# Performance work log

Hardware: AMD Instinct MI355X
Metric: run time of the kernel (lower is better)

Reference implementation:

```python
import jax, jax.numpy as jnp
import numpy as np

H = 8      # head_nums
D = 64     # head_planes
SCALE = D ** -0.5


def setup_inputs() -> dict:
    key = jax.random.key(0)
    ks = jax.random.split(key, 7)
    B, Nq, Nkv = 2, 2048, 2048
    Cq, Ck, I = 1024, 768, H * D
    return {
        "x": jax.random.normal(ks[0], (B, Nq, Cq), jnp.float32),
        "context": jax.random.normal(ks[1], (B, Nkv, Ck), jnp.float32),
        "Wq": jax.random.normal(ks[2], (Cq, I), jnp.float32) * (Cq ** -0.5),
        "Wk": jax.random.normal(ks[3], (Ck, I), jnp.float32) * (Ck ** -0.5),
        "Wv": jax.random.normal(ks[4], (Ck, I), jnp.float32) * (Ck ** -0.5),
        "Wo": jax.random.normal(ks[5], (I, Cq), jnp.float32) * (I ** -0.5),
        "bo": jnp.zeros((Cq,), jnp.float32),
    }


def reference(x, context, Wq, Wk, Wv, Wo, bo):
    B, Nq, _ = x.shape
    Nkv = context.shape[1]
    # projections (bias-free, as in to_q/to_k/to_v)
    q = (x @ Wq).reshape(B, Nq, H, D)        # b i h d
    k = (context @ Wk).reshape(B, Nkv, H, D)  # b j h d
    v = (context @ Wv).reshape(B, Nkv, H, D)
    # scaled dot-product attention, full [B,H,Nq,Nkv] scores as in original
    sim = jnp.einsum('bihd,bjhd->bhij', q, k) * SCALE
    attn = jax.nn.softmax(sim, axis=-1)
    out = jnp.einsum('bhij,bjhd->bihd', attn, v).reshape(B, Nq, H * D)
    # to_out linear (dropout_prob=0.0 -> identity)
    return out @ Wo + bo
```

## Files before the change

kernel.cpp:

```cpp
#include <hip/hip_runtime.h>
#include <hip/hip_bf16.h>

typedef __hip_bfloat16 bf16;
typedef __attribute__((ext_vector_type(8))) short short8;
typedef __attribute__((ext_vector_type(4))) float f32x4;

#define MFMA16(a, b, c) __builtin_amdgcn_mfma_f32_16x16x32_bf16((a), (b), (c), 0, 0, 0)

#define BATCH 2
#define NQ 2048
#define NKV 2048
#define HEADS 8
#define DHEAD 64
#define CQ 1024
#define CK 768
#define IDIM 512
#define SCALE 0.125f

__device__ __forceinline__ short8 ld8(const bf16* p) {
    return *(const short8*)p;
}

__device__ __forceinline__ void async_ld16(const bf16* g, bf16* l) {
    __builtin_amdgcn_global_load_lds((__attribute__((address_space(1))) const void*)g,
                                     (__attribute__((address_space(3))) void*)l,
                                     16, 0, 0);
}

__global__ __launch_bounds__(256) void prologue(
    const float* __restrict__ x, const float* __restrict__ ctx,
    const float* __restrict__ Wq, const float* __restrict__ Wk,
    const float* __restrict__ Wv, const float* __restrict__ Wo,
    bf16* __restrict__ Xb, bf16* __restrict__ Cb,
    bf16* __restrict__ WqT, bf16* __restrict__ WkT,
    bf16* __restrict__ WvT, bf16* __restrict__ WoT) {
    __shared__ float tile[64][65];
    const int t = threadIdx.x;
    const int bx = blockIdx.x;

    if (bx < 3584) {
        int idx = bx * 256 + t;
        const int NX8 = (4096 * 1024) / 8;
        const float4* srcp;
        bf16* dstp;
        if (idx < NX8) {
            srcp = (const float4*)x + (size_t)idx * 2;
            dstp = Xb + (size_t)idx * 8;
        } else {
            int j = idx - NX8;
            srcp = (const float4*)ctx + (size_t)j * 2;
            dstp = Cb + (size_t)j * 8;
        }
        float4 v0 = srcp[0], v1 = srcp[1];
        bf16 tmp[8] = {__float2bfloat16(v0.x), __float2bfloat16(v0.y),
                       __float2bfloat16(v0.z), __float2bfloat16(v0.w),
                       __float2bfloat16(v1.x), __float2bfloat16(v1.y),
                       __float2bfloat16(v1.z), __float2bfloat16(v1.w)};
        *(short8*)dstp = *(short8*)tmp;
        return;
    }

    int tb = bx - 3584;
    const float* src; bf16* dst; int R, C, ti;
    if (tb < 128)      { src = Wq; dst = WqT; R = 1024; C = 512;  ti = tb; }
    else if (tb < 224) { src = Wk; dst = WkT; R = 768;  C = 512;  ti = tb - 128; }
    else if (tb < 320) { src = Wv; dst = WvT; R = 768;  C = 512;  ti = tb - 224; }
    else               { src = Wo; dst = WoT; R = 512;  C = 1024; ti = tb - 320; }
    const int tilesC = C >> 6;
    const int tr = ti / tilesC, tc = ti - tr * tilesC;

    {
        int row = t >> 4;
        int c4 = (t & 15) * 4;
#pragma unroll
        for (int p = 0; p < 4; ++p) {
            float4 v = *(const float4*)&src[(size_t)(tr * 64 + p * 16 + row) * C + tc * 64 + c4];
            tile[p * 16 + row][c4 + 0] = v.x;
            tile[p * 16 + row][c4 + 1] = v.y;
            tile[p * 16 + row][c4 + 2] = v.z;
            tile[p * 16 + row][c4 + 3] = v.w;
        }
    }
    __syncthreads();
    {
        int oc = t >> 2;
        int r0 = (t & 3) * 16;
        bf16 tmp[16];
#pragma unroll
        for (int j = 0; j < 16; ++j)
            tmp[j] = __float2bfloat16(tile[r0 + j][oc]);
        bf16* dp = dst + (size_t)(tc * 64 + oc) * R + tr * 64 + r0;
        *(short8*)dp = *(short8*)&tmp[0];
        *(short8*)(dp + 8) = *(short8*)&tmp[8];
    }
}

__global__ __launch_bounds__(256) void qkv_gemm(
    const bf16* __restrict__ Xb, const bf16* __restrict__ Cb,
    const bf16* __restrict__ WqT, const bf16* __restrict__ WkT,
    const bf16* __restrict__ WvT,
    bf16* __restrict__ Qb, bf16* __restrict__ Kb, bf16* __restrict__ Vt) {
    __shared__ bf16 At[2][64 * 64];
    __shared__ bf16 Bts[2][128 * 64];

    const int z = blockIdx.z;
    const bf16* A  = (z == 0) ? Xb : Cb;
    const bf16* Bt = (z == 0) ? WqT : (z == 1) ? WkT : WvT;
    const int K = (z == 0) ? 1024 : 768;

    const int t = threadIdx.x;
    const int wave = t >> 6;
    const int lane = t & 63;
    const int n15 = lane & 15;
    const int quad = lane >> 4;
    const int wm = wave >> 1;
    const int wn = wave & 1;
    const int bm = blockIdx.y;
    const int bn = blockIdx.x;

    f32x4 acc[2][4] = {};

    const bf16* Ablk = A + (size_t)bm * 64 * K;
    const bf16* Bblk = Bt + (size_t)bn * 128 * K;

    int ar[2], ac[2], br[4], bc[4];
#pragma unroll
    for (int i = 0; i < 2; ++i) {
        int g = i * 256 + t;
        ar[i] = g >> 3; ac[i] = ((g & 7) ^ (ar[i] & 7)) * 8;
    }
#pragma unroll
    for (int i = 0; i < 4; ++i) {
        int g = i * 256 + t;
        br[i] = g >> 3; bc[i] = ((g & 7) ^ (br[i] & 7)) * 8;
    }

#pragma unroll
    for (int i = 0; i < 2; ++i)
        async_ld16(Ablk + ar[i] * K + ac[i], &At[0][(i * 256 + t) * 8]);
#pragma unroll
    for (int i = 0; i < 4; ++i)
        async_ld16(Bblk + br[i] * K + bc[i], &Bts[0][(i * 256 + t) * 8]);
    __syncthreads();

    for (int k0 = 0; k0 < K; k0 += 64) {
        const int p = (k0 >> 6) & 1;
        if (k0 + 64 < K) {
            const int q = p ^ 1;
            const int kn = k0 + 64;
#pragma unroll
            for (int i = 0; i < 2; ++i)
                async_ld16(Ablk + ar[i] * K + kn + ac[i], &At[q][(i * 256 + t) * 8]);
#pragma unroll
            for (int i = 0; i < 4; ++i)
                async_ld16(Bblk + br[i] * K + kn + bc[i], &Bts[q][(i * 256 + t) * 8]);
        }

#pragma unroll
        for (int kh = 0; kh < 2; ++kh) {
            short8 af[2], bfr[4];
#pragma unroll
            for (int mt = 0; mt < 2; ++mt) {
                int R = wm * 32 + mt * 16 + n15;
                af[mt] = ld8(&At[p][R * 64 + (((kh * 4 + quad) ^ (R & 7)) * 8)]);
            }
#pragma unroll
            for (int nt = 0; nt < 4; ++nt) {
                int R = wn * 64 + nt * 16 + n15;
                bfr[nt] = ld8(&Bts[p][R * 64 + (((kh * 4 + quad) ^ (R & 7)) * 8)]);
            }
#pragma unroll
            for (int mt = 0; mt < 2; ++mt)
#pragma unroll
                for (int nt = 0; nt < 4; ++nt)
                    acc[mt][nt] = MFMA16(af[mt], bfr[nt], acc[mt][nt]);
        }

        __syncthreads();
    }

    bf16* C = (z == 0) ? Qb : (z == 1) ? Kb : Vt;
#pragma unroll
    for (int mt = 0; mt < 2; ++mt) {
#pragma unroll
        for (int nt = 0; nt < 4; ++nt) {
            int col = bn * 128 + wn * 64 + nt * 16 + n15;
#pragma unroll
            for (int r = 0; r < 4; ++r) {
                int row = bm * 64 + wm * 32 + mt * 16 + quad * 4 + r;
                bf16 v = __float2bfloat16(acc[mt][nt][r]);
                if (z < 2) {
                    C[(size_t)row * 512 + col] = v;
                } else {
                    int b = row >> 11, j = row & 2047;
                    int h = col >> 6, d = col & 63;
                    C[(size_t)(((b << 3) + h) * 64 + d) * 2048 + j] = v;
                }
            }
        }
    }
}

__global__ __launch_bounds__(256) void out_gemm(const bf16* __restrict__ A,
                                                const bf16* __restrict__ Bt,
                                                const float* __restrict__ bias,
                                                float* __restrict__ C) {
    const int K = 512, N = 1024;
    __shared__ bf16 At[2][64 * 64];
    __shared__ bf16 Bts[2][128 * 64];

    const int t = threadIdx.x;
    const int wave = t >> 6;
    const int lane = t & 63;
    const int n15 = lane & 15;
    const int quad = lane >> 4;
    const int wm = wave >> 1;
    const int wn = wave & 1;
    const int bm = blockIdx.y;
    const int bn = blockIdx.x;

    f32x4 acc[2][4] = {};

    const bf16* Ablk = A + (size_t)bm * 64 * K;
    const bf16* Bblk = Bt + (size_t)bn * 128 * K;

    int ar[2], ac[2], br[4], bc[4];
#pragma unroll
    for (int i = 0; i < 2; ++i) {
        int g = i * 256 + t;
        ar[i] = g >> 3; ac[i] = ((g & 7) ^ (ar[i] & 7)) * 8;
    }
#pragma unroll
    for (int i = 0; i < 4; ++i) {
        int g = i * 256 + t;
        br[i] = g >> 3; bc[i] = ((g & 7) ^ (br[i] & 7)) * 8;
    }

#pragma unroll
    for (int i = 0; i < 2; ++i)
        async_ld16(Ablk + ar[i] * K + ac[i], &At[0][(i * 256 + t) * 8]);
#pragma unroll
    for (int i = 0; i < 4; ++i)
        async_ld16(Bblk + br[i] * K + bc[i], &Bts[0][(i * 256 + t) * 8]);
    __syncthreads();

    for (int k0 = 0; k0 < K; k0 += 64) {
        const int p = (k0 >> 6) & 1;
        if (k0 + 64 < K) {
            const int q = p ^ 1;
            const int kn = k0 + 64;
#pragma unroll
            for (int i = 0; i < 2; ++i)
                async_ld16(Ablk + ar[i] * K + kn + ac[i], &At[q][(i * 256 + t) * 8]);
#pragma unroll
            for (int i = 0; i < 4; ++i)
                async_ld16(Bblk + br[i] * K + kn + bc[i], &Bts[q][(i * 256 + t) * 8]);
        }

#pragma unroll
        for (int kh = 0; kh < 2; ++kh) {
            short8 af[2], bfr[4];
#pragma unroll
            for (int mt = 0; mt < 2; ++mt) {
                int R = wm * 32 + mt * 16 + n15;
                af[mt] = ld8(&At[p][R * 64 + (((kh * 4 + quad) ^ (R & 7)) * 8)]);
            }
#pragma unroll
            for (int nt = 0; nt < 4; ++nt) {
                int R = wn * 64 + nt * 16 + n15;
                bfr[nt] = ld8(&Bts[p][R * 64 + (((kh * 4 + quad) ^ (R & 7)) * 8)]);
            }
#pragma unroll
            for (int mt = 0; mt < 2; ++mt)
#pragma unroll
                for (int nt = 0; nt < 4; ++nt)
                    acc[mt][nt] = MFMA16(af[mt], bfr[nt], acc[mt][nt]);
        }

        __syncthreads();
    }

#pragma unroll
    for (int mt = 0; mt < 2; ++mt) {
#pragma unroll
        for (int nt = 0; nt < 4; ++nt) {
            int col = bn * 128 + wn * 64 + nt * 16 + n15;
            float bv = bias[col];
#pragma unroll
            for (int r = 0; r < 4; ++r) {
                int row = bm * 64 + wm * 32 + mt * 16 + quad * 4 + r;
                C[(size_t)row * N + col] = acc[mt][nt][r] + bv;
            }
        }
    }
}

__global__ __launch_bounds__(256, 1) void flash_attn(const bf16* __restrict__ Q,
                                                     const bf16* __restrict__ K,
                                                     const bf16* __restrict__ Vt,
                                                     bf16* __restrict__ O) {
    __shared__ bf16 Kt[2][64 * 64];
    __shared__ bf16 Vte[2][64 * 64];
    __shared__ bf16 Pa[4][32 * 72];

    const int t = threadIdx.x;
    const int wave = t >> 6;
    const int lane = t & 63;
    const int n15 = lane & 15;
    const int quad = lane >> 4;

    const int L = blockIdx.x;
    const int bh = L & 15;
    const int b = bh >> 3, h = bh & 7;
    const int q0 = (L >> 4) * 128;
    const int qw = q0 + wave * 32;

    const bf16* Qp = Q + ((size_t)(b * NQ + qw) * IDIM + h * DHEAD);
    const bf16* Kp = K + ((size_t)b * NKV * IDIM + h * DHEAD);
    const bf16* Vp = Vt + (size_t)((b * HEADS + h) * DHEAD) * NKV;
    bf16* Pw = Pa[wave];

    short8 qa[2][2];
#pragma unroll
    for (int j = 0; j < 2; ++j)
#pragma unroll
        for (int kh = 0; kh < 2; ++kh)
            qa[j][kh] = ld8(Qp + (j * 16 + n15) * IDIM + kh * 32 + quad * 8);

    const int s0 = wave * 128 + lane;
    const int s1 = s0 + 64;
    const int r0 = s0 >> 3, c0 = (s0 & 7) ^ (r0 & 7);
    const int r1 = s1 >> 3, c1 = (s1 & 7) ^ (r1 & 7);
    const bf16* kg0 = Kp + r0 * IDIM + c0 * 8;
    const bf16* kg1 = Kp + r1 * IDIM + c1 * 8;
    const bf16* vg0 = Vp + (size_t)r0 * NKV + c0 * 8;
    const bf16* vg1 = Vp + (size_t)r1 * NKV + c1 * 8;

    f32x4 o[4][2] = {};
    float lsum[2] = {0.f, 0.f};
    const int sw = n15 & 7;

    async_ld16(kg0, &Kt[0][s0 * 8]);
    async_ld16(kg1, &Kt[0][s1 * 8]);
    async_ld16(vg0, &Vte[0][s0 * 8]);
    async_ld16(vg1, &Vte[0][s1 * 8]);
    __syncthreads();

    for (int key0 = 0; key0 < NKV; key0 += 64) {
        const int p = (key0 >> 6) & 1;
        if (key0 + 64 < NKV) {
            const int q = p ^ 1;
            const int kn = key0 + 64;
            async_ld16(kg0 + (size_t)kn * IDIM, &Kt[q][s0 * 8]);
            async_ld16(kg1 + (size_t)kn * IDIM, &Kt[q][s1 * 8]);
            async_ld16(vg0 + kn, &Vte[q][s0 * 8]);
            async_ld16(vg1 + kn, &Vte[q][s1 * 8]);
        }

        f32x4 s[4][2] = {};
#pragma unroll
        for (int su = 0; su < 4; ++su) {
            const bf16* kr = &Kt[p][(su * 16 + n15) * 64];
            short8 ka0 = ld8(kr + ((quad ^ sw) * 8));
            short8 ka1 = ld8(kr + (((4 + quad) ^ sw) * 8));
#pragma unroll
            for (int j = 0; j < 2; ++j) {
                s[su][j] = MFMA16(ka0, qa[j][0], s[su][j]);
                s[su][j] = MFMA16(ka1, qa[j][1], s[su][j]);
            }
        }

#pragma unroll
        for (int su = 0; su < 4; ++su) {
#pragma unroll
            for (int j = 0; j < 2; ++j) {
                float p0 = __expf(s[su][j][0] * SCALE);
                float p1 = __expf(s[su][j][1] * SCALE);
                float p2 = __expf(s[su][j][2] * SCALE);
                float p3 = __expf(s[su][j][3] * SCALE);
                lsum[j] += (p0 + p1) + (p2 + p3);
                bf16 pk[4] = {__float2bfloat16(p0), __float2bfloat16(p1),
                              __float2bfloat16(p2), __float2bfloat16(p3)};
                *(uint2*)&Pw[(j * 16 + n15) * 72 + su * 16 + quad * 4] = *(uint2*)pk;
            }
        }
        asm volatile("s_waitcnt lgkmcnt(0)" ::: "memory");

        short8 pb[2][2];
#pragma unroll
        for (int j = 0; j < 2; ++j) {
            pb[j][0] = ld8(&Pw[(j * 16 + n15) * 72 + quad * 8]);
            pb[j][1] = ld8(&Pw[(j * 16 + n15) * 72 + 32 + quad * 8]);
        }

#pragma unroll
        for (int d4 = 0; d4 < 4; ++d4) {
            const bf16* vr = &Vte[p][(d4 * 16 + n15) * 64];
            short8 va0 = ld8(vr + ((quad ^ sw) * 8));
            short8 va1 = ld8(vr + (((4 + quad) ^ sw) * 8));
#pragma unroll
            for (int j = 0; j < 2; ++j) {
                o[d4][j] = MFMA16(va0, pb[j][0], o[d4][j]);
                o[d4][j] = MFMA16(va1, pb[j][1], o[d4][j]);
            }
        }
        __syncthreads();
    }

#pragma unroll
    for (int j = 0; j < 2; ++j) {
        float lt = lsum[j];
        lt += __shfl_xor(lt, 16, 64);
        lt += __shfl_xor(lt, 32, 64);
        float inv = 1.0f / lt;
#pragma unroll
        for (int d4 = 0; d4 < 4; ++d4) {
            bf16 pk[4];
#pragma unroll
            for (int r = 0; r < 4; ++r)
                pk[r] = __float2bfloat16(o[d4][j][r] * inv);
            *(uint2*)&Pw[(j * 16 + n15) * 72 + d4 * 16 + quad * 4] = *(uint2*)pk;
        }
    }
    __syncthreads();

    {
        int ql = t >> 1, seg = t & 1;
        const bf16* src = &Pa[ql >> 5][(ql & 31) * 72 + seg * 32];
        short8 a0 = ld8(src);
        short8 a1 = ld8(src + 8);
        short8 a2 = ld8(src + 16);
        short8 a3 = ld8(src + 24);
        bf16* dst = O + ((size_t)(b * NQ + q0 + ql) * IDIM + h * DHEAD + seg * 32);
        *(short8*)dst = a0;
        *(short8*)(dst + 8) = a1;
        *(short8*)(dst + 16) = a2;
        *(short8*)(dst + 24) = a3;
    }
}

extern "C" void kernel_launch(void* const* d_in, const int* in_sizes, int n_in,
                              void* d_out, int out_size, void* d_ws, size_t ws_size,
                              hipStream_t stream) {
    (void)in_sizes; (void)n_in; (void)out_size; (void)ws_size;

    const float* x   = (const float*)d_in[0];
    const float* ctx = (const float*)d_in[1];
    const float* Wq  = (const float*)d_in[2];
    const float* Wk  = (const float*)d_in[3];
    const float* Wv  = (const float*)d_in[4];
    const float* Wo  = (const float*)d_in[5];
    const float* bo  = (const float*)d_in[6];
    float* out = (float*)d_out;

    char* ws = (char*)d_ws;
    bf16* Xb  = (bf16*)(ws + 0);
    bf16* Cb  = (bf16*)(ws + 8388608);
    bf16* WqT = (bf16*)(ws + 14680064);
    bf16* WkT = (bf16*)(ws + 15728640);
    bf16* WvT = (bf16*)(ws + 16515072);
    bf16* WoT = (bf16*)(ws + 17301504);
    bf16* Qb  = (bf16*)(ws + 18350080);
    bf16* Kb  = (bf16*)(ws + 22544384);
    bf16* Vt  = (bf16*)(ws + 26738688);
    bf16* Ob  = (bf16*)(ws + 30932992);

    prologue<<<4032, 256, 0, stream>>>(x, ctx, Wq, Wk, Wv, Wo,
                                       Xb, Cb, WqT, WkT, WvT, WoT);

    qkv_gemm<<<dim3(4, 64, 3), 256, 0, stream>>>(Xb, Cb, WqT, WkT, WvT, Qb, Kb, Vt);

    flash_attn<<<256, 256, 0, stream>>>(Qb, Kb, Vt, Ob);

    out_gemm<<<dim3(8, 64), 256, 0, stream>>>(Ob, WoT, bo, out);
}
```

Before: 167.0 us.

## Split attention keys across wave pairs and double the flash-attention grid

Flash attention now runs 512 blocks of 512 threads. Each block covers 64 queries, and each pair of waves splits the 2048 keys into two halves. Their partial outputs and row sums are merged through shared memory before normalisation. The aim is to double the parallelism and the waves resident per CU for this small grid. The cost is losing the double-buffered K/V prefetch (each tile now loads and then synchronises), halving the reuse of each K/V fragment per wave, and adding a cross-wave reduction step.

Result: faster. 149.2 us (-10.7%).

```diff
diff --git a/kernel.cpp b/kernel.cpp
--- a/kernel.cpp
+++ b/kernel.cpp
@@ -295,16 +295,20 @@
     }
 }
 
-__global__ __launch_bounds__(256, 1) void flash_attn(const bf16* __restrict__ Q,
+__global__ __launch_bounds__(512, 1) void flash_attn(const bf16* __restrict__ Q,
                                                      const bf16* __restrict__ K,
                                                      const bf16* __restrict__ Vt,
                                                      bf16* __restrict__ O) {
     __shared__ bf16 Kt[2][64 * 64];
     __shared__ bf16 Vte[2][64 * 64];
-    __shared__ bf16 Pa[4][32 * 72];
+    __shared__ bf16 Pa[8][16 * 72];
+    __shared__ float Oc[4][64][16];
+    __shared__ float Lc[4][16];
 
     const int t = threadIdx.x;
     const int wave = t >> 6;
+    const int g = wave >> 1;
+    const int khalf = wave & 1;
     const int lane = t & 63;
     const int n15 = lane & 15;
     const int quad = lane >> 4;
@@ -312,22 +316,19 @@
     const int L = blockIdx.x;
     const int bh = L & 15;
     const int b = bh >> 3, h = bh & 7;
-    const int q0 = (L >> 4) * 128;
-    const int qw = q0 + wave * 32;
+    const int q0 = (L >> 4) * 64;
+    const int qw = q0 + g * 16;
 
     const bf16* Qp = Q + ((size_t)(b * NQ + qw) * IDIM + h * DHEAD);
-    const bf16* Kp = K + ((size_t)b * NKV * IDIM + h * DHEAD);
-    const bf16* Vp = Vt + (size_t)((b * HEADS + h) * DHEAD) * NKV;
+    const bf16* Kp = K + ((size_t)b * NKV * IDIM + h * DHEAD)
+                       + (size_t)(khalf * 1024) * IDIM;
+    const bf16* Vp = Vt + (size_t)((b * HEADS + h) * DHEAD) * NKV + khalf * 1024;
     bf16* Pw = Pa[wave];
 
-    short8 qa[2][2];
-#pragma unroll
-    for (int j = 0; j < 2; ++j)
-#pragma unroll
-        for (int kh = 0; kh < 2; ++kh)
-            qa[j][kh] = ld8(Qp + (j * 16 + n15) * IDIM + kh * 32 + quad * 8);
-
-    const int s0 = wave * 128 + lane;
+    short8 qa0 = ld8(Qp + n15 * IDIM + quad * 8);
+    short8 qa1 = ld8(Qp + n15 * IDIM + 32 + quad * 8);
+
+    const int s0 = g * 128 + lane;
     const int s1 = s0 + 64;
     const int r0 = s0 >> 3, c0 = (s0 & 7) ^ (r0 & 7);
     const int r1 = s1 >> 3, c1 = (s1 & 7) ^ (r1 & 7);
@@ -335,107 +336,93 @@
     const bf16* kg1 = Kp + r1 * IDIM + c1 * 8;
     const bf16* vg0 = Vp + (size_t)r0 * NKV + c0 * 8;
     const bf16* vg1 = Vp + (size_t)r1 * NKV + c1 * 8;
-
-    f32x4 o[4][2] = {};
-    float lsum[2] = {0.f, 0.f};
+    bf16* kl0 = &Kt[khalf][s0 * 8];
+    bf16* kl1 = &Kt[khalf][s1 * 8];
+    bf16* vl0 = &Vte[khalf][s0 * 8];
+    bf16* vl1 = &Vte[khalf][s1 * 8];
+
+    f32x4 o[4] = {};
+    float lsum = 0.f;
     const int sw = n15 & 7;
 
-    async_ld16(kg0, &Kt[0][s0 * 8]);
-    async_ld16(kg1, &Kt[0][s1 * 8]);
-    async_ld16(vg0, &Vte[0][s0 * 8]);
-    async_ld16(vg1, &Vte[0][s1 * 8]);
-    __syncthreads();
-
-    for (int key0 = 0; key0 < NKV; key0 += 64) {
-        const int p = (key0 >> 6) & 1;
-        if (key0 + 64 < NKV) {
-            const int q = p ^ 1;
-            const int kn = key0 + 64;
-            async_ld16(kg0 + (size_t)kn * IDIM, &Kt[q][s0 * 8]);
-            async_ld16(kg1 + (size_t)kn * IDIM, &Kt[q][s1 * 8]);
-            async_ld16(vg0 + kn, &Vte[q][s0 * 8]);
-            async_ld16(vg1 + kn, &Vte[q][s1 * 8]);
-        }
-
-        f32x4 s[4][2] = {};
+    for (int key0 = 0; key0 < 1024; key0 += 64) {
+        async_ld16(kg0 + (size_t)key0 * IDIM, kl0);
+        async_ld16(kg1 + (size_t)key0 * IDIM, kl1);
+        async_ld16(vg0 + key0, vl0);
+        async_ld16(vg1 + key0, vl1);
+        __syncthreads();
+
+        f32x4 s[4] = {};
 #pragma unroll
         for (int su = 0; su < 4; ++su) {
-            const bf16* kr = &Kt[p][(su * 16 + n15) * 64];
+            const bf16* kr = &Kt[khalf][(su * 16 + n15) * 64];
             short8 ka0 = ld8(kr + ((quad ^ sw) * 8));
             short8 ka1 = ld8(kr + (((4 + quad) ^ sw) * 8));
-#pragma unroll
-            for (int j = 0; j < 2; ++j) {
-                s[su][j] = MFMA16(ka0, qa[j][0], s[su][j]);
-                s[su][j] = MFMA16(ka1, qa[j][1], s[su][j]);
-            }
+            s[su] = MFMA16(ka0, qa0, s[su]);
+            s[su] = MFMA16(ka1, qa1, s[su]);
         }
 
 #pragma unroll
         for (int su = 0; su < 4; ++su) {
-#pragma unroll
-            for (int j = 0; j < 2; ++j) {
-                float p0 = __expf(s[su][j][0] * SCALE);
-                float p1 = __expf(s[su][j][1] * SCALE);
-                float p2 = __expf(s[su][j][2] * SCALE);
-                float p3 = __expf(s[su][j][3] * SCALE);
-                lsum[j] += (p0 + p1) + (p2 + p3);
-                bf16 pk[4] = {__float2bfloat16(p0), __float2bfloat16(p1),
-                              __float2bfloat16(p2), __float2bfloat16(p3)};
-                *(uint2*)&Pw[(j * 16 + n15) * 72 + su * 16 + quad * 4] = *(uint2*)pk;
-            }
+            float p0 = __expf(s[su][0] * SCALE);
+            float p1 = __expf(s[su][1] * SCALE);
+            float p2 = __expf(s[su][2] * SCALE);
+            float p3 = __expf(s[su][3] * SCALE);
+            lsum += (p0 + p1) + (p2 + p3);
+            bf16 pk[4] = {__float2bfloat16(p0), __float2bfloat16(p1),
+                          __float2bfloat16(p2), __float2bfloat16(p3)};
+            *(uint2*)&Pw[n15 * 72 + su * 16 + quad * 4] = *(uint2*)pk;
         }
         asm volatile("s_waitcnt lgkmcnt(0)" ::: "memory");
 
-        short8 pb[2][2];
-#pragma unroll
-        for (int j = 0; j < 2; ++j) {
-            pb[j][0] = ld8(&Pw[(j * 16 + n15) * 72 + quad * 8]);
-            pb[j][1] = ld8(&Pw[(j * 16 + n15) * 72 + 32 + quad * 8]);
-        }
+        short8 pb0 = ld8(&Pw[n15 * 72 + quad * 8]);
+        short8 pb1 = ld8(&Pw[n15 * 72 + 32 + quad * 8]);
 
 #pragma unroll
         for (int d4 = 0; d4 < 4; ++d4) {
-            const bf16* vr = &Vte[p][(d4 * 16 + n15) * 64];
+            const bf16* vr = &Vte[khalf][(d4 * 16 + n15) * 64];
             short8 va0 = ld8(vr + ((quad ^ sw) * 8));
             short8 va1 = ld8(vr + (((4 + quad) ^ sw) * 8));
-#pragma unroll
-            for (int j = 0; j < 2; ++j) {
-                o[d4][j] = MFMA16(va0, pb[j][0], o[d4][j]);
-                o[d4][j] = MFMA16(va1, pb[j][1], o[d4][j]);
-            }
+            o[d4] = MFMA16(va0, pb0, o[d4]);
+            o[d4] = MFMA16(va1, pb1, o[d4]);
         }
         __syncthreads();
     }
 
-#pragma unroll
-    for (int j = 0; j < 2; ++j) {
-        float lt = lsum[j];
-        lt += __shfl_xor(lt, 16, 64);
-        lt += __shfl_xor(lt, 32, 64);
+    lsum += __shfl_xor(lsum, 16, 64);
+    lsum += __shfl_xor(lsum, 32, 64);
+
+    if (khalf == 1) {
+#pragma unroll
+        for (int d4 = 0; d4 < 4; ++d4)
+#pragma unroll
+            for (int r = 0; r < 4; ++r)
+                Oc[g][d4 * 16 + quad * 4 + r][n15] = o[d4][r];
+        if (quad == 0) Lc[g][n15] = lsum;
+    }
+    __syncthreads();
+    if (khalf == 0) {
+        float lt = lsum + Lc[g][n15];
         float inv = 1.0f / lt;
 #pragma unroll
         for (int d4 = 0; d4 < 4; ++d4) {
             bf16 pk[4];
 #pragma unroll
-            for (int r = 0; r < 4; ++r)
-                pk[r] = __float2bfloat16(o[d4][j][r] * inv);
-            *(uint2*)&Pw[(j * 16 + n15) * 72 + d4 * 16 + quad * 4] = *(uint2*)pk;
+            for (int r = 0; r < 4; ++r) {
+                float v = o[d4][r] + Oc[g][d4 * 16 + quad * 4 + r][n15];
+                pk[r] = __float2bfloat16(v * inv);
+            }
+            *(uint2*)&Pa[g][n15 * 72 + d4 * 16 + quad * 4] = *(uint2*)pk;
         }
     }
     __syncthreads();
 
     {
-        int ql = t >> 1, seg = t & 1;
-        const bf16* src = &Pa[ql >> 5][(ql & 31) * 72 + seg * 32];
+        int ql = t >> 3, seg = t & 7;
+        const bf16* src = &Pa[ql >> 4][(ql & 15) * 72 + seg * 8];
         short8 a0 = ld8(src);
-        short8 a1 = ld8(src + 8);
-        short8 a2 = ld8(src + 16);
-        short8 a3 = ld8(src + 24);
-        bf16* dst = O + ((size_t)(b * NQ + q0 + ql) * IDIM + h * DHEAD + seg * 32);
+        bf16* dst = O + ((size_t)(b * NQ + q0 + ql) * IDIM + h * DHEAD + seg * 8);
         *(short8*)dst = a0;
-        *(short8*)(dst + 8) = a1;
-        *(short8*)(dst + 16) = a2;
-        *(short8*)(dst + 24) = a3;
     }
 }
 
@@ -470,7 +457,7 @@
 
     qkv_gemm<<<dim3(4, 64, 3), 256, 0, stream>>>(Xb, Cb, WqT, WkT, WvT, Qb, Kb, Vt);
 
-    flash_attn<<<256, 256, 0, stream>>>(Qb, Kb, Vt, Ob);
+    flash_attn<<<512, 512, 0, stream>>>(Qb, Kb, Vt, Ob);
 
     out_gemm<<<dim3(8, 64), 256, 0, stream>>>(Ob, WoT, bo, out);
 }
```
